# Optimization experiments

Measured on AMD Instinct MI355X. Metric: run time of the kernel, lower is better.

Reference implementation:

```python
import jax, jax.numpy as jnp
import numpy as np

HS_ENC, HS_DEC, ATTN = 1024, 1024, 1024
N, T = 32, 2048


def setup_inputs() -> dict:
    key = jax.random.key(0)
    k1, k2, k3, k4, k5, k6 = jax.random.split(key, 6)
    h_dec = jax.random.normal(k1, (N, HS_DEC), dtype=jnp.float32)
    h_enc = jax.random.normal(k2, (N, T, HS_ENC), dtype=jnp.float32)
    src_lens = jax.random.randint(k3, (N,), 1, T + 1, dtype=jnp.int32)
    # params of nn.Linear(hs_enc+hs_dec, attn_size) and score vector v
    W = jax.random.normal(k4, (ATTN, HS_DEC + HS_ENC), dtype=jnp.float32) * 0.02
    b = jax.random.normal(k5, (ATTN,), dtype=jnp.float32) * 0.02
    v = jax.random.normal(k6, (ATTN,), dtype=jnp.float32)
    return {"h_dec": h_dec, "h_enc": h_enc, "src_lens": src_lens, "W": W, "b": b, "v": v}


def reference(h_dec, h_enc, src_lens, W, b, v):
    # Linear over concat(h_dec, h_enc) == sum of split projections; avoids
    # materializing the repeated/concatenated [N, T, hs_dec+hs_enc] tensor.
    hs_dec = h_dec.shape[-1]
    Wd, We = W[:, :hs_dec], W[:, hs_dec:]          # [A, hs_dec], [A, hs_enc]
    dec_proj = jnp.einsum('nd,ad->na', h_dec, Wd)  # [N, A]
    enc_proj = jnp.einsum('nte,ae->nta', h_enc, We)  # [N, T, A]
    attn_out = jnp.tanh(dec_proj[:, None, :] + enc_proj + b)  # [N, T, A]
    score = jnp.einsum('nta,a->nt', attn_out, v)   # [N, T]
    T_ = h_enc.shape[1]
    mask = jnp.arange(T_)[None, :] < src_lens[:, None]
    score = jnp.where(mask, score, jnp.float32(-1e10))
    weights = jax.nn.softmax(score, axis=-1)       # [N, T]
    ctx = jnp.einsum('nt,nte->ne', weights, h_enc) # [N, hs_enc]
    return ctx, weights
```

## Files before the change

### kernel.cpp

```cpp
#include <hip/hip_runtime.h>
#include <hip/hip_fp16.h>

#define HS 1024
#define TT 2048

typedef _Float16 half8 __attribute__((ext_vector_type(8)));
typedef float floatx4 __attribute__((ext_vector_type(4)));

__device__ __forceinline__ void dma16(const _Float16* g, _Float16* l) {
    __builtin_amdgcn_global_load_lds(
        (const __attribute__((address_space(1))) unsigned int*)g,
        (__attribute__((address_space(3))) unsigned int*)l, 16, 0, 0);
}

__global__ __launch_bounds__(256) void k_dproj(const float* __restrict__ h_dec,
                                               const float* __restrict__ W,
                                               const float* __restrict__ bias,
                                               float* __restrict__ dproj) {
    int wid = blockIdx.x * 4 + (threadIdx.x >> 6);
    int lane = threadIdx.x & 63;
    int n = wid >> 10, a = wid & 1023;
    const float4* hd = reinterpret_cast<const float4*>(h_dec + (size_t)n * HS);
    const float4* wr = reinterpret_cast<const float4*>(W + (size_t)a * 2048);
    float s = 0.f;
#pragma unroll
    for (int i = 0; i < 4; ++i) {
        float4 h = hd[lane + i * 64];
        float4 w = wr[lane + i * 64];
        s += h.x * w.x + h.y * w.y + h.z * w.z + h.w * w.w;
    }
    for (int off = 32; off; off >>= 1) s += __shfl_xor(s, off);
    if (lane == 0) dproj[wid] = bias[a] + s;
}

__global__ __launch_bounds__(256) void k_cvtW(const float* __restrict__ W,
                                              _Float16* __restrict__ We16) {
    int idx4 = (blockIdx.x * 256 + threadIdx.x) * 4;
    int a = idx4 >> 10;
    int e = idx4 & 1023;
    float4 f = *reinterpret_cast<const float4*>(W + (size_t)a * 2048 + 1024 + e);
    _Float16 h0 = (_Float16)f.x, h1 = (_Float16)f.y, h2 = (_Float16)f.z, h3 = (_Float16)f.w;
    ushort4 p;
    p.x = *(unsigned short*)&h0; p.y = *(unsigned short*)&h1;
    p.z = *(unsigned short*)&h2; p.w = *(unsigned short*)&h3;
    *reinterpret_cast<ushort4*>(We16 + idx4) = p;
}

__global__ __launch_bounds__(256) void k_cvtA(const float* __restrict__ h_enc,
                                              _Float16* __restrict__ h_enc16) {
    size_t idx = ((size_t)blockIdx.x * 256 + threadIdx.x) * 16;
    const float4* g = reinterpret_cast<const float4*>(h_enc + idx);
    _Float16 h[16];
#pragma unroll
    for (int i = 0; i < 4; ++i) {
        float4 f = g[i];
        h[i * 4 + 0] = (_Float16)f.x; h[i * 4 + 1] = (_Float16)f.y;
        h[i * 4 + 2] = (_Float16)f.z; h[i * 4 + 3] = (_Float16)f.w;
    }
    *reinterpret_cast<uint4*>(h_enc16 + idx)     = *reinterpret_cast<uint4*>(&h[0]);
    *reinterpret_cast<uint4*>(h_enc16 + idx + 8) = *reinterpret_cast<uint4*>(&h[8]);
}

__global__ __launch_bounds__(256, 2) void k_score(const _Float16* __restrict__ h_enc16,
                                                  const _Float16* __restrict__ We16,
                                                  const float* __restrict__ dproj,
                                                  const float* __restrict__ v,
                                                  float* __restrict__ scores) {
    __shared__ _Float16 Asb[2][128 * 32];
    __shared__ _Float16 Bsb[2][256 * 32];
    __shared__ float s_acc[128];

    const int tid = threadIdx.x;
    const int n  = blockIdx.x >> 4;
    const int t0 = (blockIdx.x & 15) << 7;

    if (tid < 128) s_acc[tid] = 0.0f;

    const int w    = tid >> 6;
    const int lane = tid & 63;
    const int wm = w >> 1, wn = w & 1;
    const int col = lane & 15, quad = lane >> 4;

    const int lrow = lane >> 2;
    const int lg   = (lane & 3) ^ ((lrow >> 1) & 3);
    const size_t goff = (size_t)lrow * HS + lg * 8;

    const _Float16* gA = h_enc16 + (size_t)(n * TT + t0) * HS + goff;
    const _Float16* gB = We16 + goff;

    floatx4 acc[4][8];
    float vv[8], dd[8];

    auto issue = [&](int it, int p) {
        const int a0 = (it >> 5) << 8;
        const int kk = (it & 31) << 5;
        const _Float16* gAi = gA + kk;
        const _Float16* gBi = gB + (size_t)a0 * HS + kk;
#pragma unroll
        for (int j = 0; j < 2; ++j)
            dma16(gAi + (size_t)(w * 32 + j * 16) * HS, &Asb[p][(w * 2 + j) * 512]);
#pragma unroll
        for (int j = 0; j < 4; ++j)
            dma16(gBi + (size_t)(w * 64 + j * 16) * HS, &Bsb[p][(w * 4 + j) * 512]);
    };

    issue(0, 0);

    for (int it = 0; it < 128; ++it) {
        const int p = it & 1;

        __syncthreads();

        if (it + 1 < 128) issue(it + 1, 1 - p);

        if ((it & 31) == 0) {
            const int a0 = (it >> 5) << 8;
#pragma unroll
            for (int ni = 0; ni < 8; ++ni) {
                int a = a0 + wn * 128 + ni * 16 + col;
                vv[ni] = v[a];
                dd[ni] = dproj[n * HS + a];
            }
#pragma unroll
            for (int mi = 0; mi < 4; ++mi)
#pragma unroll
                for (int ni = 0; ni < 8; ++ni)
                    acc[mi][ni] = (floatx4)0.0f;
        }

        const _Float16* Ab = Asb[p];
        const _Float16* Bb = Bsb[p];
        half8 af[4], bf[8];
#pragma unroll
        for (int mi = 0; mi < 4; ++mi) {
            const int r = wm * 64 + mi * 16 + col;
            af[mi] = *reinterpret_cast<const half8*>(
                &Ab[r * 32 + ((quad ^ ((r >> 1) & 3)) << 3)]);
        }
#pragma unroll
        for (int ni = 0; ni < 8; ++ni) {
            const int r = wn * 128 + ni * 16 + col;
            bf[ni] = *reinterpret_cast<const half8*>(
                &Bb[r * 32 + ((quad ^ ((r >> 1) & 3)) << 3)]);
        }
#pragma unroll
        for (int mi = 0; mi < 4; ++mi)
#pragma unroll
            for (int ni = 0; ni < 8; ++ni)
                acc[mi][ni] = __builtin_amdgcn_mfma_f32_16x16x32_f16(
                    af[mi], bf[ni], acc[mi][ni], 0, 0, 0);

        if ((it & 31) == 31) {
#pragma unroll
            for (int mi = 0; mi < 4; ++mi) {
#pragma unroll
                for (int rg = 0; rg < 4; ++rg) {
                    float s = 0.0f;
#pragma unroll
                    for (int ni = 0; ni < 8; ++ni) {
                        float x = acc[mi][ni][rg] + dd[ni];
                        float e2 = __expf(2.0f * x);
                        float th = 1.0f - 2.0f * __builtin_amdgcn_rcpf(e2 + 1.0f);
                        s += vv[ni] * th;
                    }
                    s += __shfl_xor(s, 8);
                    s += __shfl_xor(s, 4);
                    s += __shfl_xor(s, 2);
                    s += __shfl_xor(s, 1);
                    if (col == 0)
                        atomicAdd(&s_acc[wm * 64 + mi * 16 + quad * 4 + rg], s);
                }
            }
        }
    }
    __syncthreads();
    if (tid < 128) scores[(size_t)n * TT + t0 + tid] = s_acc[tid];
}

__global__ __launch_bounds__(256) void k_softmax(float* __restrict__ wout,
                                                 const int* __restrict__ lens) {
    __shared__ float red[4];
    __shared__ float red2[4];
    int n = blockIdx.x, tid = threadIdx.x;
    int len = lens[n];
    float* row = wout + (size_t)n * TT;
    float sv[8];
    float m = -3.0e38f;
#pragma unroll
    for (int i = 0; i < 8; ++i) {
        int t = tid + i * 256;
        float s = row[t];
        s = (t < len) ? s : -1.0e10f;
        sv[i] = s;
        m = fmaxf(m, s);
    }
    for (int off = 1; off <= 32; off <<= 1) m = fmaxf(m, __shfl_xor(m, off));
    if ((tid & 63) == 0) red[tid >> 6] = m;
    __syncthreads();
    m = fmaxf(fmaxf(red[0], red[1]), fmaxf(red[2], red[3]));
    float sum = 0.f, es[8];
#pragma unroll
    for (int i = 0; i < 8; ++i) { es[i] = __expf(sv[i] - m); sum += es[i]; }
    for (int off = 1; off <= 32; off <<= 1) sum += __shfl_xor(sum, off);
    if ((tid & 63) == 0) red2[tid >> 6] = sum;
    __syncthreads();
    sum = red2[0] + red2[1] + red2[2] + red2[3];
    float rinv = 1.0f / sum;
#pragma unroll
    for (int i = 0; i < 8; ++i) row[tid + i * 256] = es[i] * rinv;
}

__global__ __launch_bounds__(256) void k_ctx(const _Float16* __restrict__ h_enc16,
                                             const float* __restrict__ wts,
                                             float* __restrict__ ctx) {
    __shared__ float red[256][8];
    int b = blockIdx.x;
    int n  = b >> 4;
    int ec = (b >> 2) & 3;
    int ts = b & 3;
    int tid = threadIdx.x;
    int q = tid & 31, tg = tid >> 5;
    int e = ec * 256 + q * 8;
    float acc[8];
#pragma unroll
    for (int j = 0; j < 8; ++j) acc[j] = 0.f;
    const float* wrow = wts + (size_t)n * TT;
    for (int t = ts * 512 + tg; t < ts * 512 + 512; t += 8) {
        float w = wrow[t];
        uint4 raw = *reinterpret_cast<const uint4*>(
            h_enc16 + ((size_t)(n * TT + t)) * HS + e);
        const _Float16* hp = reinterpret_cast<const _Float16*>(&raw);
#pragma unroll
        for (int j = 0; j < 8; ++j) acc[j] += w * (float)hp[j];
    }
#pragma unroll
    for (int j = 0; j < 8; ++j) red[tid][j] = acc[j];
    __syncthreads();
    if (tid < 32) {
        float s[8];
#pragma unroll
        for (int j = 0; j < 8; ++j) s[j] = red[tid][j];
        for (int g = 1; g < 8; ++g)
#pragma unroll
            for (int j = 0; j < 8; ++j) s[j] += red[g * 32 + tid][j];
        float* dst = ctx + (size_t)n * HS + ec * 256 + tid * 8;
#pragma unroll
        for (int j = 0; j < 8; ++j) atomicAdd(dst + j, s[j]);
    }
}

__global__ __launch_bounds__(256) void k_score_naive(const float* __restrict__ h_enc,
                                                     const float* __restrict__ W,
                                                     const float* __restrict__ dproj,
                                                     const float* __restrict__ v,
                                                     float* __restrict__ scores) {
    int gw = blockIdx.x * 4 + (threadIdx.x >> 6);
    int lane = threadIdx.x & 63;
    int n = gw >> 11, t = gw & 2047;
    const float4* he = reinterpret_cast<const float4*>(h_enc + ((size_t)(n * TT + t)) * HS);
    float4 hv[4];
#pragma unroll
    for (int i = 0; i < 4; ++i) hv[i] = he[lane + i * 64];
    float s = 0.f;
    for (int a = 0; a < 1024; ++a) {
        const float4* wr = reinterpret_cast<const float4*>(W + (size_t)a * 2048 + 1024);
        float d = 0.f;
#pragma unroll
        for (int i = 0; i < 4; ++i) {
            float4 wv = wr[lane + i * 64];
            d += hv[i].x * wv.x + hv[i].y * wv.y + hv[i].z * wv.z + hv[i].w * wv.w;
        }
        for (int off = 32; off; off >>= 1) d += __shfl_xor(d, off);
        s += v[a] * tanhf(d + dproj[n * HS + a]);
    }
    if (lane == 0) scores[(size_t)n * TT + t] = s;
}

__global__ __launch_bounds__(256) void k_ctx_naive(const float* __restrict__ h_enc,
                                                   const float* __restrict__ wts,
                                                   float* __restrict__ ctx) {
    int n = blockIdx.x;
    int e = threadIdx.x * 4;
    float4 a = make_float4(0.f, 0.f, 0.f, 0.f);
    const float* wrow = wts + (size_t)n * TT;
    for (int t = 0; t < TT; ++t) {
        float w = wrow[t];
        float4 h = *reinterpret_cast<const float4*>(h_enc + ((size_t)(n * TT + t)) * HS + e);
        a.x += w * h.x; a.y += w * h.y; a.z += w * h.z; a.w += w * h.w;
    }
    *reinterpret_cast<float4*>(ctx + (size_t)n * HS + e) = a;
}

extern "C" void kernel_launch(void* const* d_in, const int* in_sizes, int n_in,
                              void* d_out, int out_size, void* d_ws, size_t ws_size,
                              hipStream_t stream) {
    const float* h_dec    = (const float*)d_in[0];
    const float* h_enc    = (const float*)d_in[1];
    const int*   src_lens = (const int*)d_in[2];
    const float* W = (const float*)d_in[3];
    const float* b = (const float*)d_in[4];
    const float* v = (const float*)d_in[5];

    float* out = (float*)d_out;
    float* ctx = out;
    float* wts = out + 32 * 1024;

    float*    dproj   = (float*)d_ws;
    _Float16* We16    = (_Float16*)((char*)d_ws + 131072);
    _Float16* h_enc16 = (_Float16*)((char*)d_ws + 131072 + 2097152);
    const size_t need = 131072 + 2097152 + (size_t)32 * TT * HS * 2;

    k_dproj<<<8192, 256, 0, stream>>>(h_dec, W, b, dproj);
    if (ws_size >= need) {
        (void)hipMemsetAsync(ctx, 0, 32 * 1024 * sizeof(float), stream);
        k_cvtW <<<1024, 256, 0, stream>>>(W, We16);
        k_cvtA <<<16384, 256, 0, stream>>>(h_enc, h_enc16);
        k_score<<<512, 256, 0, stream>>>(h_enc16, We16, dproj, v, wts);
        k_softmax<<<32, 256, 0, stream>>>(wts, src_lens);
        k_ctx  <<<512, 256, 0, stream>>>(h_enc16, wts, ctx);
    } else {
        k_score_naive<<<16384, 256, 0, stream>>>(h_enc, W, dproj, v, wts);
        k_softmax<<<32, 256, 0, stream>>>(wts, src_lens);
        k_ctx_naive<<<32, 256, 0, stream>>>(h_enc, wts, ctx);
    }
}
```

Baseline: 592.8 us.

## Triple-buffer score GEMM loads, merge prep kernels, pad ctx reduction buffer

The score GEMM moves from double to triple LDS buffering. It waits with explicit vmcnt and a raw barrier so two tiles stay in flight, and it restructures the loop into four passes with the epilogue outside the k-loop. The dproj and weight-conversion kernels merge into one launch to save a launch. The fp16 cast kernel now handles 8 elements per thread, and the ctx reduction buffer is transposed and padded to avoid LDS bank conflicts. Triple buffering raises LDS use, which may lower occupancy. The hand-written waitcnt assumes a fixed count of outstanding loads per thread.

Result: slower. 635.6 us (+7.2%).

```diff
diff --git a/kernel.cpp b/kernel.cpp
--- a/kernel.cpp
+++ b/kernel.cpp
@@ -13,52 +13,50 @@
         (__attribute__((address_space(3))) unsigned int*)l, 16, 0, 0);
 }
 
-__global__ __launch_bounds__(256) void k_dproj(const float* __restrict__ h_dec,
-                                               const float* __restrict__ W,
-                                               const float* __restrict__ bias,
-                                               float* __restrict__ dproj) {
-    int wid = blockIdx.x * 4 + (threadIdx.x >> 6);
-    int lane = threadIdx.x & 63;
-    int n = wid >> 10, a = wid & 1023;
-    const float4* hd = reinterpret_cast<const float4*>(h_dec + (size_t)n * HS);
-    const float4* wr = reinterpret_cast<const float4*>(W + (size_t)a * 2048);
-    float s = 0.f;
-#pragma unroll
-    for (int i = 0; i < 4; ++i) {
-        float4 h = hd[lane + i * 64];
-        float4 w = wr[lane + i * 64];
-        s += h.x * w.x + h.y * w.y + h.z * w.z + h.w * w.w;
-    }
-    for (int off = 32; off; off >>= 1) s += __shfl_xor(s, off);
-    if (lane == 0) dproj[wid] = bias[a] + s;
-}
-
-__global__ __launch_bounds__(256) void k_cvtW(const float* __restrict__ W,
+__global__ __launch_bounds__(256) void k_prep(const float* __restrict__ h_dec,
+                                              const float* __restrict__ W,
+                                              const float* __restrict__ bias,
+                                              float* __restrict__ dproj,
                                               _Float16* __restrict__ We16) {
-    int idx4 = (blockIdx.x * 256 + threadIdx.x) * 4;
-    int a = idx4 >> 10;
-    int e = idx4 & 1023;
-    float4 f = *reinterpret_cast<const float4*>(W + (size_t)a * 2048 + 1024 + e);
-    _Float16 h0 = (_Float16)f.x, h1 = (_Float16)f.y, h2 = (_Float16)f.z, h3 = (_Float16)f.w;
-    ushort4 p;
-    p.x = *(unsigned short*)&h0; p.y = *(unsigned short*)&h1;
-    p.z = *(unsigned short*)&h2; p.w = *(unsigned short*)&h3;
-    *reinterpret_cast<ushort4*>(We16 + idx4) = p;
+    int b = blockIdx.x;
+    if (b < 8192) {
+        int wid = b * 4 + (threadIdx.x >> 6);
+        int lane = threadIdx.x & 63;
+        int n = wid >> 10, a = wid & 1023;
+        const float4* hd = reinterpret_cast<const float4*>(h_dec + (size_t)n * HS);
+        const float4* wr = reinterpret_cast<const float4*>(W + (size_t)a * 2048);
+        float s = 0.f;
+#pragma unroll
+        for (int i = 0; i < 4; ++i) {
+            float4 h = hd[lane + i * 64];
+            float4 w = wr[lane + i * 64];
+            s += h.x * w.x + h.y * w.y + h.z * w.z + h.w * w.w;
+        }
+        for (int off = 32; off; off >>= 1) s += __shfl_xor(s, off);
+        if (lane == 0) dproj[wid] = bias[a] + s;
+    } else {
+        int idx4 = ((b - 8192) * 256 + threadIdx.x) * 4;
+        int a = idx4 >> 10;
+        int e = idx4 & 1023;
+        float4 f = *reinterpret_cast<const float4*>(W + (size_t)a * 2048 + 1024 + e);
+        _Float16 h0 = (_Float16)f.x, h1 = (_Float16)f.y;
+        _Float16 h2 = (_Float16)f.z, h3 = (_Float16)f.w;
+        ushort4 p;
+        p.x = *(unsigned short*)&h0; p.y = *(unsigned short*)&h1;
+        p.z = *(unsigned short*)&h2; p.w = *(unsigned short*)&h3;
+        *reinterpret_cast<ushort4*>(We16 + idx4) = p;
+    }
 }
 
 __global__ __launch_bounds__(256) void k_cvtA(const float* __restrict__ h_enc,
                                               _Float16* __restrict__ h_enc16) {
-    size_t idx = ((size_t)blockIdx.x * 256 + threadIdx.x) * 16;
+    size_t idx = ((size_t)blockIdx.x * 256 + threadIdx.x) * 8;
     const float4* g = reinterpret_cast<const float4*>(h_enc + idx);
-    _Float16 h[16];
-#pragma unroll
-    for (int i = 0; i < 4; ++i) {
-        float4 f = g[i];
-        h[i * 4 + 0] = (_Float16)f.x; h[i * 4 + 1] = (_Float16)f.y;
-        h[i * 4 + 2] = (_Float16)f.z; h[i * 4 + 3] = (_Float16)f.w;
-    }
-    *reinterpret_cast<uint4*>(h_enc16 + idx)     = *reinterpret_cast<uint4*>(&h[0]);
-    *reinterpret_cast<uint4*>(h_enc16 + idx + 8) = *reinterpret_cast<uint4*>(&h[8]);
+    float4 f0 = g[0], f1 = g[1];
+    _Float16 h[8];
+    h[0] = (_Float16)f0.x; h[1] = (_Float16)f0.y; h[2] = (_Float16)f0.z; h[3] = (_Float16)f0.w;
+    h[4] = (_Float16)f1.x; h[5] = (_Float16)f1.y; h[6] = (_Float16)f1.z; h[7] = (_Float16)f1.w;
+    *reinterpret_cast<uint4*>(h_enc16 + idx) = *reinterpret_cast<uint4*>(&h[0]);
 }
 
 __global__ __launch_bounds__(256, 2) void k_score(const _Float16* __restrict__ h_enc16,
@@ -66,8 +64,8 @@
                                                   const float* __restrict__ dproj,
                                                   const float* __restrict__ v,
                                                   float* __restrict__ scores) {
-    __shared__ _Float16 Asb[2][128 * 32];
-    __shared__ _Float16 Bsb[2][256 * 32];
+    __shared__ _Float16 Asb[3][128 * 32];
+    __shared__ _Float16 Bsb[3][256 * 32];
     __shared__ float s_acc[128];
 
     const int tid = threadIdx.x;
@@ -89,11 +87,10 @@
     const _Float16* gB = We16 + goff;
 
     floatx4 acc[4][8];
-    float vv[8], dd[8];
-
-    auto issue = [&](int it, int p) {
-        const int a0 = (it >> 5) << 8;
-        const int kk = (it & 31) << 5;
+
+    auto issue = [&](int src, int p) {
+        const int a0 = (src >> 5) << 8;
+        const int kk = (src & 31) << 5;
         const _Float16* gAi = gA + kk;
         const _Float16* gBi = gB + (size_t)a0 * HS + kk;
 #pragma unroll
@@ -105,52 +102,59 @@
     };
 
     issue(0, 0);
-
-    for (int it = 0; it < 128; ++it) {
-        const int p = it & 1;
-
-        __syncthreads();
-
-        if (it + 1 < 128) issue(it + 1, 1 - p);
-
-        if ((it & 31) == 0) {
-            const int a0 = (it >> 5) << 8;
+    issue(1, 1);
+
+    for (int pass = 0; pass < 4; ++pass) {
+#pragma unroll
+        for (int mi = 0; mi < 4; ++mi)
+#pragma unroll
+            for (int ni = 0; ni < 8; ++ni)
+                acc[mi][ni] = (floatx4)0.0f;
+
+        for (int kit = 0; kit < 32; ++kit) {
+            const int it = pass * 32 + kit;
+            const int p = it % 3;
+
+            asm volatile("s_waitcnt vmcnt(6)" ::: "memory");
+            asm volatile("s_barrier" ::: "memory");
+
+            {
+                const int nx = it + 2;
+                issue(nx < 128 ? nx : 127, nx % 3);
+            }
+
+            const _Float16* Ab = Asb[p];
+            const _Float16* Bb = Bsb[p];
+            half8 af[4], bf[8];
+#pragma unroll
+            for (int mi = 0; mi < 4; ++mi) {
+                const int r = wm * 64 + mi * 16 + col;
+                af[mi] = *reinterpret_cast<const half8*>(
+                    &Ab[r * 32 + ((quad ^ ((r >> 1) & 3)) << 3)]);
+            }
+#pragma unroll
+            for (int ni = 0; ni < 8; ++ni) {
+                const int r = wn * 128 + ni * 16 + col;
+                bf[ni] = *reinterpret_cast<const half8*>(
+                    &Bb[r * 32 + ((quad ^ ((r >> 1) & 3)) << 3)]);
+            }
+#pragma unroll
+            for (int mi = 0; mi < 4; ++mi)
+#pragma unroll
+                for (int ni = 0; ni < 8; ++ni)
+                    acc[mi][ni] = __builtin_amdgcn_mfma_f32_16x16x32_f16(
+                        af[mi], bf[ni], acc[mi][ni], 0, 0, 0);
+        }
+
+        {
+            const int a0 = pass << 8;
+            float vv[8], dd[8];
 #pragma unroll
             for (int ni = 0; ni < 8; ++ni) {
                 int a = a0 + wn * 128 + ni * 16 + col;
                 vv[ni] = v[a];
                 dd[ni] = dproj[n * HS + a];
             }
-#pragma unroll
-            for (int mi = 0; mi < 4; ++mi)
-#pragma unroll
-                for (int ni = 0; ni < 8; ++ni)
-                    acc[mi][ni] = (floatx4)0.0f;
-        }
-
-        const _Float16* Ab = Asb[p];
-        const _Float16* Bb = Bsb[p];
-        half8 af[4], bf[8];
-#pragma unroll
-        for (int mi = 0; mi < 4; ++mi) {
-            const int r = wm * 64 + mi * 16 + col;
-            af[mi] = *reinterpret_cast<const half8*>(
-                &Ab[r * 32 + ((quad ^ ((r >> 1) & 3)) << 3)]);
-        }
-#pragma unroll
-        for (int ni = 0; ni < 8; ++ni) {
-            const int r = wn * 128 + ni * 16 + col;
-            bf[ni] = *reinterpret_cast<const half8*>(
-                &Bb[r * 32 + ((quad ^ ((r >> 1) & 3)) << 3)]);
-        }
-#pragma unroll
-        for (int mi = 0; mi < 4; ++mi)
-#pragma unroll
-            for (int ni = 0; ni < 8; ++ni)
-                acc[mi][ni] = __builtin_amdgcn_mfma_f32_16x16x32_f16(
-                    af[mi], bf[ni], acc[mi][ni], 0, 0, 0);
-
-        if ((it & 31) == 31) {
 #pragma unroll
             for (int mi = 0; mi < 4; ++mi) {
 #pragma unroll
@@ -213,7 +217,7 @@
 __global__ __launch_bounds__(256) void k_ctx(const _Float16* __restrict__ h_enc16,
                                              const float* __restrict__ wts,
                                              float* __restrict__ ctx) {
-    __shared__ float red[256][8];
+    __shared__ float red[8][257];
     int b = blockIdx.x;
     int n  = b >> 4;
     int ec = (b >> 2) & 3;
@@ -234,15 +238,15 @@
         for (int j = 0; j < 8; ++j) acc[j] += w * (float)hp[j];
     }
 #pragma unroll
-    for (int j = 0; j < 8; ++j) red[tid][j] = acc[j];
+    for (int j = 0; j < 8; ++j) red[j][tid] = acc[j];
     __syncthreads();
     if (tid < 32) {
         float s[8];
 #pragma unroll
-        for (int j = 0; j < 8; ++j) s[j] = red[tid][j];
+        for (int j = 0; j < 8; ++j) s[j] = red[j][tid];
         for (int g = 1; g < 8; ++g)
 #pragma unroll
-            for (int j = 0; j < 8; ++j) s[j] += red[g * 32 + tid][j];
+            for (int j = 0; j < 8; ++j) s[j] += red[j][g * 32 + tid];
         float* dst = ctx + (size_t)n * HS + ec * 256 + tid * 8;
 #pragma unroll
         for (int j = 0; j < 8; ++j) atomicAdd(dst + j, s[j]);
@@ -310,15 +314,15 @@
     _Float16* h_enc16 = (_Float16*)((char*)d_ws + 131072 + 2097152);
     const size_t need = 131072 + 2097152 + (size_t)32 * TT * HS * 2;
 
-    k_dproj<<<8192, 256, 0, stream>>>(h_dec, W, b, dproj);
     if (ws_size >= need) {
         (void)hipMemsetAsync(ctx, 0, 32 * 1024 * sizeof(float), stream);
-        k_cvtW <<<1024, 256, 0, stream>>>(W, We16);
-        k_cvtA <<<16384, 256, 0, stream>>>(h_enc, h_enc16);
+        k_prep<<<9216, 256, 0, stream>>>(h_dec, W, b, dproj, We16);
+        k_cvtA<<<32768, 256, 0, stream>>>(h_enc, h_enc16);
         k_score<<<512, 256, 0, stream>>>(h_enc16, We16, dproj, v, wts);
         k_softmax<<<32, 256, 0, stream>>>(wts, src_lens);
-        k_ctx  <<<512, 256, 0, stream>>>(h_enc16, wts, ctx);
+        k_ctx<<<512, 256, 0, stream>>>(h_enc16, wts, ctx);
     } else {
+        k_prep<<<9216, 256, 0, stream>>>(h_dec, W, b, dproj, We16);
         k_score_naive<<<16384, 256, 0, stream>>>(h_enc, W, dproj, v, wts);
         k_softmax<<<32, 256, 0, stream>>>(wts, src_lens);
         k_ctx_naive<<<32, 256, 0, stream>>>(h_enc, wts, ctx);
```
